# Performance work log

Measured on AMD Instinct MI355X. Metric: run time of the kernel, lower is better.

Reference implementation:

```python
import jax, jax.numpy as jnp
import numpy as np

# Per-species MLP dims from CoefficientLayer._create_model (H, C, N, O), aev_dim=384
DIMS = {"h": [384, 160, 128, 96, 1], "c": [384, 144, 112, 96, 1], "n": [384, 128, 112, 96, 1], "o": [384, 128, 112, 96, 1]}


def setup_inputs() -> dict:
    key = jax.random.key(0)
    B, A, D = 256, 256, 384
    ks = jax.random.split(key, 64)
    inp = {}
    inp["species"] = jax.random.randint(ks[0], (B, A), 0, 4)  # species index 0..3
    inp["aev"] = jax.random.normal(ks[1], (B, A, D), dtype=jnp.float32)
    inp["b0"] = jnp.array([0.1, 0.2, 0.3, 0.4], dtype=jnp.float32)  # shifter intercepts
    inp["b1"] = jnp.array([1.0, 1.1, 0.9, 1.2], dtype=jnp.float32)  # shifter slopes
    ki = 2
    for name, dims in DIMS.items():
        for l in range(4):
            fi, fo = dims[l], dims[l + 1]
            inp[f"{name}w{l}"] = jax.random.normal(ks[ki], (fi, fo), dtype=jnp.float32) / np.float32(np.sqrt(fi))
            ki += 1
            inp[f"{name}b{l}"] = jnp.zeros((fo,), dtype=jnp.float32)
    return inp


def _mlp(x, ws, bs):
    # Linear -> CELU(0.1) x3 -> Linear(->1), squeeze last dim
    for i in range(3):
        x = jax.nn.celu(x @ ws[i] + bs[i], alpha=0.1)
    return (x @ ws[3] + bs[3])[..., 0]


def reference(species, aev, b0, b1,
              hw0, hb0, hw1, hb1, hw2, hb2, hw3, hb3,
              cw0, cb0, cw1, cb1, cw2, cb2, cw3, cb3,
              nw0, nb0, nw1, nb1, nw2, nb2, nw3, nb3,
              ow0, ob0, ow1, ob1, ow2, ob2, ow3, ob3):
    nets = [
        ([hw0, hw1, hw2, hw3], [hb0, hb1, hb2, hb3]),
        ([cw0, cw1, cw2, cw3], [cb0, cb1, cb2, cb3]),
        ([nw0, nw1, nw2, nw3], [nb0, nb1, nb2, nb3]),
        ([ow0, ow1, ow2, ow3], [ob0, ob1, ob2, ob3]),
    ]
    # ANIModel hard routing: each atom's coefficient comes from its species' network;
    # atoms with species == -1 (padding) stay 0.
    coef = jnp.zeros(species.shape, dtype=aev.dtype)
    for i, (ws, bs) in enumerate(nets):  # fixed small loop over 4 species
        coef = jnp.where(species == i, _mlp(aev, ws, bs), coef)
    # Shifter: result[mask_i] = b0[i] + b1[i] * coef[mask_i]; padding stays 0
    idx = jnp.clip(species, 0)
    return jnp.where(species >= 0, b0[idx] + b1[idx] * coef, jnp.zeros((), dtype=aev.dtype))
```

## Files before the change

kernel.cpp:

```cpp
#include <hip/hip_runtime.h>

typedef _Float16 f16;
typedef _Float16 f16x4 __attribute__((ext_vector_type(4)));
typedef _Float16 f16x8 __attribute__((ext_vector_type(8)));
typedef float f32x4 __attribute__((ext_vector_type(4)));
typedef unsigned short u16;
typedef unsigned int u32;

#define NATOMS 65536
#define CAP 17920

#define WS_LISTS_OFF 256
#define WS_W_OFF 524544
#define WS_W_ELEMS 350208
#define WS_ACT0_OFF (2u << 20)
#define WS_BIG (46u << 20)

#define BLK0 128
#define BLK12 64

#define ROWB 1536
#define ROWH 768
#define TILEH 12288

struct ConvJob { const float* src; int K, N, KS, NT, CK, off; };

struct PrepParams {
  const int* species;
  int* counts;
  u16* lists;
  f16* wbase;
  ConvJob jobs[16];
};

struct GemmParams {
  const float* aev;
  const float* b0;
  const float* b1;
  const float* bias[4][4];
  const float* w3src[4];
  const f16* w[4][4];
  const int* counts;
  const u16* lists;
  f16* act0;
  float* out;
  int Nreal0[4];
  int Nreal1[4];
};

template <int N> struct AF { f16x8 v[N]; };

__global__ __launch_bounds__(256) void prep_kernel(PrepParams p) {
  int tid = threadIdx.x;
  if (blockIdx.x < 256) {
    __shared__ int wcnt[4][4];
    __shared__ int wbase[4][4];
    int i = blockIdx.x * 256 + tid;
    int s = p.species[i];
    int wave = tid >> 6, lane = tid & 63;
    unsigned long long m[4];
    #pragma unroll
    for (int t = 0; t < 4; t++) {
      m[t] = __ballot(s == t);
      if (lane == 0) wcnt[wave][t] = __popcll(m[t]);
    }
    __syncthreads();
    if (tid < 4) {
      int t = tid;
      int c0 = wcnt[0][t], c1 = wcnt[1][t], c2 = wcnt[2][t], c3 = wcnt[3][t];
      int base = atomicAdd(&p.counts[t], c0 + c1 + c2 + c3);
      wbase[0][t] = base;
      wbase[1][t] = base + c0;
      wbase[2][t] = base + c0 + c1;
      wbase[3][t] = base + c0 + c1 + c2;
    }
    __syncthreads();
    int rnk = __popcll(m[s] & ((1ull << lane) - 1ull));
    p.lists[s * NATOMS + wbase[wave][s] + rnk] = (u16)i;
  } else {
    int bx = blockIdx.x - 256;
    int job = bx / 30, bxin = bx - job * 30;
    ConvJob jb = p.jobs[job];
    int e = bxin * 256 + tid;
    int nslots = jb.KS * jb.NT * 64;
    if (e >= nslots) return;
    int frag = e >> 6, lane = e & 63;
    int c = frag / (jb.CK * jb.NT);
    int rem = frag - c * (jb.CK * jb.NT);
    int ckc = min(jb.CK, jb.KS - c * jb.CK);
    int nt = rem / ckc, ki = rem - nt * ckc;
    int ks = c * jb.CK + ki;
    int q = lane >> 4, nlo = lane & 15;
    int n = nt * 16 + nlo;
    int k0 = ks * 32 + q * 8;
    f16x8 v;
    #pragma unroll
    for (int j = 0; j < 8; j++) {
      int k = k0 + j;
      float x = (n < jb.N && k < jb.K) ? jb.src[k * jb.N + n] : 0.f;
      v[j] = (f16)x;
    }
    *(f16x8*)(p.wbase + jb.off + (size_t)e * 8) = v;
  }
}

__device__ __forceinline__ float celu01(float v) {
  return v > 0.f ? v : 0.1f * (__expf(v * 10.f) - 1.f);
}

__device__ __forceinline__ void stage_frag(const f16* g, f16* l, int lane) {
  __builtin_amdgcn_global_load_lds(
      (const __attribute__((address_space(1))) u32*)(g + lane * 8),
      (__attribute__((address_space(3))) u32*)l, 16, 0, 0);
}

template <int NT0>
__device__ void k0_body(const GemmParams& p, int s, int bl, char* smem) {
  int tid = threadIdx.x, w = tid >> 6, lane = tid & 63;
  int q = lane >> 4, nlo = lane & 15;
  int cnt = min(p.counts[s], CAP);
  int ntiles = (cnt + 15) >> 4;
  int tpb = (ntiles + BLK0 - 1) / BLK0;
  int t0 = bl * tpb;
  int nt_blk = min(ntiles - t0, tpb);
  if (nt_blk <= 0) return;

  const u16* list = p.lists + s * NATOMS;
  u16* atoms_l = (u16*)(smem + 2 * TILEH);

  f16x8 wf[12];
  float bvv[4];
  if (w < NT0) {
    const f16* wg = p.w[s][0];
    #pragma unroll
    for (int ks = 0; ks < 12; ks++)
      wf[ks] = *(const f16x8*)(wg + (size_t)(ks * NT0 + w) * 512 + lane * 8);
    #pragma unroll
    for (int r = 0; r < 4; r++) {
      int n = w * 16 + q * 4 + r;
      bvv[r] = (n < p.Nreal0[s]) ? p.bias[s][0][n] : 0.f;
    }
  }
  f16* act = p.act0 + (size_t)s * CAP * 160;

  for (int idx = tid; idx < nt_blk * 16; idx += 640)
    atoms_l[idx] = list[min(t0 * 16 + idx, cnt - 1)];
  __syncthreads();

  bool stager = (w < 8);
  int frow[3], fintra[3];
  #pragma unroll
  for (int j = 0; j < 3; j++) {
    int o32 = (w + 8 * j) * 1024 + lane * 16;
    frow[j] = o32 / ROWB;
    fintra[j] = o32 - frow[j] * ROWB;
  }

  f32x4 ld[3];
  auto issue = [&](int i) {
    #pragma unroll
    for (int j = 0; j < 3; j++) {
      int atom = atoms_l[i * 16 + frow[j]];
      ld[j] = *(const f32x4*)((const char*)p.aev + (size_t)atom * ROWB + fintra[j]);
    }
  };
  auto write_lds = [&](int i) {
    char* buf = smem + (i & 1) * TILEH;
    #pragma unroll
    for (int j = 0; j < 3; j++) {
      int o16 = (w + 8 * j) * 512 + lane * 8;
      int addr = o16 ^ ((frow[j] & 7) << 4);
      f16x4 h = {(f16)ld[j][0], (f16)ld[j][1], (f16)ld[j][2], (f16)ld[j][3]};
      *(f16x4*)(buf + addr) = h;
    }
  };

  if (stager) {
    issue(0);
    write_lds(0);
    if (nt_blk > 1) issue(1);
  }
  asm volatile("s_waitcnt lgkmcnt(0)" ::: "memory");
  __builtin_amdgcn_s_barrier();

  for (int i = 0; i < nt_blk; i++) {
    if (stager) {
      if (i + 1 < nt_blk) write_lds(i + 1);
      if (i + 2 < nt_blk) issue(i + 2);
    }
    if (w < NT0) {
      const char* buf = smem + (i & 1) * TILEH;
      int swz = (nlo & 7) << 4;
      int base = nlo * ROWH + q * 16;
      f32x4 acc = {0.f, 0.f, 0.f, 0.f};
      #pragma unroll
      for (int ks = 0; ks < 12; ks++) {
        f16x8 a = *(const f16x8*)(buf + ((base + ks * 64) ^ swz));
        acc = __builtin_amdgcn_mfma_f32_16x16x32_f16(wf[ks], a, acc, 0, 0, 0);
      }
      int row = (t0 + i) * 16 + nlo;
      if (row < cnt) {
        f16x4 o;
        #pragma unroll
        for (int r = 0; r < 4; r++) o[r] = (f16)celu01(acc[r] + bvv[r]);
        *(f16x4*)(act + (size_t)row * 160 + w * 16 + q * 4) = o;
      }
    }
    asm volatile("s_waitcnt lgkmcnt(0)" ::: "memory");
    __builtin_amdgcn_s_barrier();
  }
}

__global__ __launch_bounds__(640, 5) void k0_kernel(GemmParams p) {
  __shared__ __align__(16) char smem[2 * TILEH + 384];
  int s = blockIdx.x & 3, bl = blockIdx.x >> 2;
  switch (s) {
    case 0: k0_body<10>(p, 0, bl, smem); break;
    case 1: k0_body<10>(p, 1, bl, smem); break;
    case 2: k0_body<8>(p, 2, bl, smem); break;
    default: k0_body<8>(p, 3, bl, smem); break;
  }
}

template <int KS1>
__device__ void k12_body(const GemmParams& p, int s, int bl, f16* W1, f16* W2,
                         f16* T) {
  int tid = threadIdx.x, w = tid >> 6, lane = tid & 63;
  int q = lane >> 4, nlo = lane & 15;
  constexpr int NF1 = KS1 * 8;
  const f16* g1 = p.w[s][1];
  const f16* g2 = p.w[s][2];
  for (int f = w; f < NF1 + 24; f += 8) {
    if (f < NF1) stage_frag(g1 + (size_t)f * 512, W1 + f * 512, lane);
    else stage_frag(g2 + (size_t)(f - NF1) * 512, W2 + (f - NF1) * 512, lane);
  }
  int cnt = min(p.counts[s], CAP);
  int ntiles = (cnt + 15) >> 4;
  const u16* list = p.lists + s * NATOMS;
  int Nr1 = p.Nreal1[s];
  const float* bias1 = p.bias[s][1];
  const float* bias2 = p.bias[s][2];
  const float* w3 = p.w3src[s];
  float bv[8], b2v[6], w3v[6];
  #pragma unroll
  for (int nt = 0; nt < 8; nt++) {
    int n = nt * 16 + nlo;
    bv[nt] = (n < Nr1) ? bias1[n] : 0.f;
  }
  #pragma unroll
  for (int nt = 0; nt < 6; nt++) {
    int n = nt * 16 + nlo;
    b2v[nt] = bias2[n];
    w3v[nt] = w3[n];
  }
  float b3 = p.bias[s][3][0];
  float b0v = p.b0[s], b1v = p.b1[s];
  const f16* act0 = p.act0 + (size_t)s * CAP * 160;
  f16* Tw = T + (w * 16) * 160;
  __syncthreads();

  auto load_a1 = [&](int t) {
    AF<KS1> a;
    int ar = min(t * 16 + nlo, cnt - 1);
    const f16* ap = act0 + (size_t)ar * 160 + q * 8;
    #pragma unroll
    for (int ks = 0; ks < KS1; ks++)
      a.v[ks] = *(const f16x8*)(ap + ks * 32);
    return a;
  };

  int t = bl * 8 + w;
  if (t >= ntiles) return;
  AF<KS1> a1 = load_a1(t);
  while (true) {
    int tn = t + BLK12 * 8;
    AF<KS1> a1n;
    if (tn < ntiles) a1n = load_a1(tn);
    int tb = t * 16;
    f32x4 acc1[8];
    #pragma unroll
    for (int nt = 0; nt < 8; nt++) acc1[nt] = f32x4{0.f, 0.f, 0.f, 0.f};
    #pragma unroll
    for (int ks = 0; ks < KS1; ks++) {
      #pragma unroll
      for (int nt = 0; nt < 8; nt++) {
        f16x8 b = *(const f16x8*)(W1 + (ks * 8 + nt) * 512 + lane * 8);
        acc1[nt] = __builtin_amdgcn_mfma_f32_16x16x32_f16(a1.v[ks], b, acc1[nt], 0, 0, 0);
      }
    }
    #pragma unroll
    for (int nt = 0; nt < 8; nt++) {
      #pragma unroll
      for (int r = 0; r < 4; r++)
        Tw[(q * 4 + r) * 160 + nt * 16 + nlo] = (f16)celu01(acc1[nt][r] + bv[nt]);
    }
    AF<4> a2;
    #pragma unroll
    for (int ks = 0; ks < 4; ks++)
      a2.v[ks] = *(const f16x8*)(Tw + nlo * 160 + ks * 32 + q * 8);
    f32x4 acc2[6];
    #pragma unroll
    for (int nt = 0; nt < 6; nt++) acc2[nt] = f32x4{0.f, 0.f, 0.f, 0.f};
    #pragma unroll
    for (int ks = 0; ks < 4; ks++) {
      #pragma unroll
      for (int nt = 0; nt < 6; nt++) {
        f16x8 b = *(const f16x8*)(W2 + (ks * 6 + nt) * 512 + lane * 8);
        acc2[nt] = __builtin_amdgcn_mfma_f32_16x16x32_f16(a2.v[ks], b, acc2[nt], 0, 0, 0);
      }
    }
    float pr[4] = {0.f, 0.f, 0.f, 0.f};
    #pragma unroll
    for (int nt = 0; nt < 6; nt++) {
      #pragma unroll
      for (int r = 0; r < 4; r++) {
        float v = celu01(acc2[nt][r] + b2v[nt]);
        pr[r] += v * w3v[nt];
      }
    }
    #pragma unroll
    for (int m = 1; m < 16; m <<= 1) {
      #pragma unroll
      for (int r = 0; r < 4; r++) pr[r] += __shfl_xor(pr[r], m);
    }
    if (nlo == 0) {
      #pragma unroll
      for (int r = 0; r < 4; r++) {
        int row = tb + q * 4 + r;
        if (row < cnt) p.out[list[row]] = b0v + b1v * (pr[r] + b3);
      }
    }
    if (tn >= ntiles) break;
    a1 = a1n;
    t = tn;
  }
}

__global__ __launch_bounds__(512, 2) void k12_kernel(GemmParams p) {
  __shared__ __align__(16) f16 W1[5 * 8 * 512];
  __shared__ __align__(16) f16 W2[4 * 6 * 512];
  __shared__ __align__(16) f16 T[8 * 16 * 160];
  int s = blockIdx.x & 3, bl = blockIdx.x >> 2;
  switch (s) {
    case 0: k12_body<5>(p, 0, bl, W1, W2, T); break;
    case 1: k12_body<5>(p, 1, bl, W1, W2, T); break;
    case 2: k12_body<4>(p, 2, bl, W1, W2, T); break;
    default: k12_body<4>(p, 3, bl, W1, W2, T); break;
  }
}


extern "C" void kernel_launch(void* const* d_in, const int* in_sizes, int n_in,
                              void* d_out, int out_size, void* d_ws, size_t ws_size,
                              hipStream_t stream) {
  if (ws_size < WS_BIG) return;

  const int* species = (const int*)d_in[0];
  const float* aev = (const float*)d_in[1];
  const float* b0 = (const float*)d_in[2];
  const float* b1 = (const float*)d_in[3];

  static const int F1[4]  = {160, 144, 128, 128};
  static const int F1p[4] = {160, 160, 128, 128};
  static const int F2[4]  = {128, 112, 112, 112};

  char* wsb = (char*)d_ws;
  int* counts = (int*)wsb;
  u16* lists = (u16*)(wsb + WS_LISTS_OFF);
  f16* wbase = (f16*)(wsb + WS_W_OFF);

  PrepParams pp;
  pp.species = species; pp.counts = counts; pp.lists = lists; pp.wbase = wbase;

  GemmParams mp;
  mp.aev = aev; mp.b0 = b0; mp.b1 = b1;
  mp.counts = counts; mp.lists = lists; mp.out = (float*)d_out;
  mp.act0 = (f16*)(wsb + WS_ACT0_OFF);

  int off = 0, ji = 0;
  for (int s = 0; s < 4; s++) {
    int K[4]  = {384, F1[s], F2[s], 96};
    int N[4]  = {F1[s], F2[s], 96, 1};
    int KS[4] = {12, F1p[s] / 32, 4, 3};
    int NT[4] = {F1p[s] / 16, 8, 6, 1};
    int CK[4] = {1, 1, 1, 3};
    for (int l = 0; l < 4; l++) {
      const float* w = (const float*)d_in[4 + s * 8 + l * 2];
      const float* b = (const float*)d_in[4 + s * 8 + l * 2 + 1];
      pp.jobs[ji].src = w;
      pp.jobs[ji].K = K[l];
      pp.jobs[ji].N = N[l];
      pp.jobs[ji].KS = KS[l];
      pp.jobs[ji].NT = NT[l];
      pp.jobs[ji].CK = CK[l];
      pp.jobs[ji].off = off;
      mp.w[s][l] = wbase + off;
      mp.bias[s][l] = b;
      off += KS[l] * NT[l] * 512;
      ji++;
    }
    mp.w3src[s] = (const float*)d_in[4 + s * 8 + 6];
    mp.Nreal0[s] = F1[s];
    mp.Nreal1[s] = F2[s];
  }

  hipMemsetAsync(d_ws, 0, 64, stream);
  prep_kernel<<<dim3(256 + 480), 256, 0, stream>>>(pp);
  k0_kernel<<<dim3(4 * BLK0), 640, 0, stream>>>(mp);
  k12_kernel<<<dim3(4 * BLK12), 512, 0, stream>>>(mp);
}
```

Before: 260.3 us.

## Fuse layer-0 GEMM with layers 1-3 into one kernel via LDS activations

Merges the layer-0 kernel and the layers-1/2/3 kernel into one kernel. Layer-0 outputs for up to 8 tiles are kept in LDS, then each wave runs the remaining MLP layers on one tile, so the fp16 activation tensor is no longer written to and read back from global memory and one launch disappears. In exchange, LDS use grows to about 130KB per block, occupancy drops, grid size halves to 64 blocks per species, and the layer-0 aev prefetch pipeline restarts every 8 tiles with extra barriers.

```diff
diff --git a/kernel.cpp b/kernel.cpp
--- a/kernel.cpp
+++ b/kernel.cpp
@@ -13,11 +13,9 @@
 #define WS_LISTS_OFF 256
 #define WS_W_OFF 524544
 #define WS_W_ELEMS 350208
-#define WS_ACT0_OFF (2u << 20)
-#define WS_BIG (46u << 20)
-
-#define BLK0 128
-#define BLK12 64
+#define WS_NEEDED (WS_W_OFF + WS_W_ELEMS * 2)
+
+#define BLKF 64
 
 #define ROWB 1536
 #define ROWH 768
@@ -42,7 +40,6 @@
   const f16* w[4][4];
   const int* counts;
   const u16* lists;
-  f16* act0;
   float* out;
   int Nreal0[4];
   int Nreal1[4];
@@ -114,19 +111,35 @@
       (__attribute__((address_space(3))) u32*)l, 16, 0, 0);
 }
 
-template <int NT0>
-__device__ void k0_body(const GemmParams& p, int s, int bl, char* smem) {
+template <int NT0, int KS1>
+__device__ void fused_body(const GemmParams& p, int s, int bl, char* smem) {
+  constexpr int LDSA_OFF = 2 * TILEH;
+  constexpr int TSTRIDE = 16 * 168;
+  constexpr int W1_OFF = LDSA_OFF + 8 * TSTRIDE * 2;
+  constexpr int W2_OFF = W1_OFF + 40 * 512 * 2;
+  constexpr int ATOMS_OFF = W2_OFF + 24 * 512 * 2;
+  constexpr int NF1 = KS1 * 8;
+
   int tid = threadIdx.x, w = tid >> 6, lane = tid & 63;
   int q = lane >> 4, nlo = lane & 15;
   int cnt = min(p.counts[s], CAP);
   int ntiles = (cnt + 15) >> 4;
-  int tpb = (ntiles + BLK0 - 1) / BLK0;
+  int tpb = (ntiles + BLKF - 1) / BLKF;
   int t0 = bl * tpb;
   int nt_blk = min(ntiles - t0, tpb);
   if (nt_blk <= 0) return;
 
-  const u16* list = p.lists + s * NATOMS;
-  u16* atoms_l = (u16*)(smem + 2 * TILEH);
+  f16* ldsA = (f16*)(smem + LDSA_OFF);
+  f16* W1 = (f16*)(smem + W1_OFF);
+  f16* W2 = (f16*)(smem + W2_OFF);
+  u16* atoms_l = (u16*)(smem + ATOMS_OFF);
+
+  const f16* g1 = p.w[s][1];
+  const f16* g2 = p.w[s][2];
+  for (int f = w; f < NF1 + 24; f += 10) {
+    if (f < NF1) stage_frag(g1 + (size_t)f * 512, W1 + f * 512, lane);
+    else stage_frag(g2 + (size_t)(f - NF1) * 512, W2 + (f - NF1) * 512, lane);
+  }
 
   f16x8 wf[12];
   float bvv[4];
@@ -141,8 +154,27 @@
       bvv[r] = (n < p.Nreal0[s]) ? p.bias[s][0][n] : 0.f;
     }
   }
-  f16* act = p.act0 + (size_t)s * CAP * 160;
-
+
+  int Nr1 = p.Nreal1[s];
+  const float* bias1 = p.bias[s][1];
+  const float* bias2 = p.bias[s][2];
+  const float* w3 = p.w3src[s];
+  float bv1[8], b2v[6], w3v[6];
+  #pragma unroll
+  for (int nt = 0; nt < 8; nt++) {
+    int n = nt * 16 + nlo;
+    bv1[nt] = (n < Nr1) ? bias1[n] : 0.f;
+  }
+  #pragma unroll
+  for (int nt = 0; nt < 6; nt++) {
+    int n = nt * 16 + nlo;
+    b2v[nt] = bias2[n];
+    w3v[nt] = w3[n];
+  }
+  float b3 = p.bias[s][3][0];
+  float b0v = p.b0[s], b1v = p.b1[s];
+
+  const u16* list = p.lists + s * NATOMS;
   for (int idx = tid; idx < nt_blk * 16; idx += 640)
     atoms_l[idx] = list[min(t0 * 16 + idx, cnt - 1)];
   __syncthreads();
@@ -175,177 +207,117 @@
     }
   };
 
-  if (stager) {
-    issue(0);
-    write_lds(0);
-    if (nt_blk > 1) issue(1);
-  }
-  asm volatile("s_waitcnt lgkmcnt(0)" ::: "memory");
-  __builtin_amdgcn_s_barrier();
-
-  for (int i = 0; i < nt_blk; i++) {
+  for (int lo = 0; lo < nt_blk; lo += 8) {
+    int hi = min(nt_blk, lo + 8);
+
     if (stager) {
-      if (i + 1 < nt_blk) write_lds(i + 1);
-      if (i + 2 < nt_blk) issue(i + 2);
-    }
-    if (w < NT0) {
-      const char* buf = smem + (i & 1) * TILEH;
-      int swz = (nlo & 7) << 4;
-      int base = nlo * ROWH + q * 16;
-      f32x4 acc = {0.f, 0.f, 0.f, 0.f};
-      #pragma unroll
-      for (int ks = 0; ks < 12; ks++) {
-        f16x8 a = *(const f16x8*)(buf + ((base + ks * 64) ^ swz));
-        acc = __builtin_amdgcn_mfma_f32_16x16x32_f16(wf[ks], a, acc, 0, 0, 0);
-      }
-      int row = (t0 + i) * 16 + nlo;
-      if (row < cnt) {
-        f16x4 o;
-        #pragma unroll
-        for (int r = 0; r < 4; r++) o[r] = (f16)celu01(acc[r] + bvv[r]);
-        *(f16x4*)(act + (size_t)row * 160 + w * 16 + q * 4) = o;
-      }
+      issue(lo);
+      write_lds(lo);
+      if (lo + 1 < hi) issue(lo + 1);
     }
     asm volatile("s_waitcnt lgkmcnt(0)" ::: "memory");
     __builtin_amdgcn_s_barrier();
-  }
-}
-
-__global__ __launch_bounds__(640, 5) void k0_kernel(GemmParams p) {
-  __shared__ __align__(16) char smem[2 * TILEH + 384];
+
+    for (int i = lo; i < hi; i++) {
+      if (stager) {
+        if (i + 1 < hi) write_lds(i + 1);
+        if (i + 2 < hi) issue(i + 2);
+      }
+      if (w < NT0) {
+        const char* buf = smem + (i & 1) * TILEH;
+        int swz = (nlo & 7) << 4;
+        int base = nlo * ROWH + q * 16;
+        f32x4 acc = {0.f, 0.f, 0.f, 0.f};
+        #pragma unroll
+        for (int ks = 0; ks < 12; ks++) {
+          f16x8 a = *(const f16x8*)(buf + ((base + ks * 64) ^ swz));
+          acc = __builtin_amdgcn_mfma_f32_16x16x32_f16(wf[ks], a, acc, 0, 0, 0);
+        }
+        f16* A = ldsA + (i - lo) * TSTRIDE;
+        f16x4 o;
+        #pragma unroll
+        for (int r = 0; r < 4; r++) o[r] = (f16)celu01(acc[r] + bvv[r]);
+        *(f16x4*)(A + nlo * 168 + w * 16 + q * 4) = o;
+      }
+      asm volatile("s_waitcnt lgkmcnt(0)" ::: "memory");
+      __builtin_amdgcn_s_barrier();
+    }
+
+    if (w < 8 && lo + w < hi) {
+      int i = lo + w;
+      f16* A = ldsA + w * TSTRIDE;
+      AF<KS1> a1;
+      #pragma unroll
+      for (int ks = 0; ks < KS1; ks++)
+        a1.v[ks] = *(const f16x8*)(A + nlo * 168 + ks * 32 + q * 8);
+      f32x4 acc1[8];
+      #pragma unroll
+      for (int nt = 0; nt < 8; nt++) acc1[nt] = f32x4{0.f, 0.f, 0.f, 0.f};
+      #pragma unroll
+      for (int ks = 0; ks < KS1; ks++) {
+        #pragma unroll
+        for (int nt = 0; nt < 8; nt++) {
+          f16x8 b = *(const f16x8*)(W1 + (ks * 8 + nt) * 512 + lane * 8);
+          acc1[nt] = __builtin_amdgcn_mfma_f32_16x16x32_f16(a1.v[ks], b, acc1[nt], 0, 0, 0);
+        }
+      }
+      #pragma unroll
+      for (int nt = 0; nt < 8; nt++) {
+        #pragma unroll
+        for (int r = 0; r < 4; r++)
+          A[(q * 4 + r) * 168 + nt * 16 + nlo] = (f16)celu01(acc1[nt][r] + bv1[nt]);
+      }
+      AF<4> a2;
+      #pragma unroll
+      for (int ks = 0; ks < 4; ks++)
+        a2.v[ks] = *(const f16x8*)(A + nlo * 168 + ks * 32 + q * 8);
+      f32x4 acc2[6];
+      #pragma unroll
+      for (int nt = 0; nt < 6; nt++) acc2[nt] = f32x4{0.f, 0.f, 0.f, 0.f};
+      #pragma unroll
+      for (int ks = 0; ks < 4; ks++) {
+        #pragma unroll
+        for (int nt = 0; nt < 6; nt++) {
+          f16x8 b = *(const f16x8*)(W2 + (ks * 6 + nt) * 512 + lane * 8);
+          acc2[nt] = __builtin_amdgcn_mfma_f32_16x16x32_f16(a2.v[ks], b, acc2[nt], 0, 0, 0);
+        }
+      }
+      float pr[4] = {0.f, 0.f, 0.f, 0.f};
+      #pragma unroll
+      for (int nt = 0; nt < 6; nt++) {
+        #pragma unroll
+        for (int r = 0; r < 4; r++) {
+          float v = celu01(acc2[nt][r] + b2v[nt]);
+          pr[r] += v * w3v[nt];
+        }
+      }
+      #pragma unroll
+      for (int m = 1; m < 16; m <<= 1) {
+        #pragma unroll
+        for (int r = 0; r < 4; r++) pr[r] += __shfl_xor(pr[r], m);
+      }
+      if (nlo == 0) {
+        #pragma unroll
+        for (int r = 0; r < 4; r++) {
+          int row = (t0 + i) * 16 + q * 4 + r;
+          if (row < cnt)
+            p.out[atoms_l[i * 16 + q * 4 + r]] = b0v + b1v * (pr[r] + b3);
+        }
+      }
+    }
+    asm volatile("s_waitcnt lgkmcnt(0)" ::: "memory");
+    __builtin_amdgcn_s_barrier();
+  }
+}
+
+__global__ __launch_bounds__(640, 2) void fused_kernel(GemmParams p) {
+  __shared__ __align__(16) char smem[133760];
   int s = blockIdx.x & 3, bl = blockIdx.x >> 2;
   switch (s) {
-    case 0: k0_body<10>(p, 0, bl, smem); break;
-    case 1: k0_body<10>(p, 1, bl, smem); break;
-    case 2: k0_body<8>(p, 2, bl, smem); break;
-    default: k0_body<8>(p, 3, bl, smem); break;
-  }
-}
-
-template <int KS1>
-__device__ void k12_body(const GemmParams& p, int s, int bl, f16* W1, f16* W2,
-                         f16* T) {
-  int tid = threadIdx.x, w = tid >> 6, lane = tid & 63;
-  int q = lane >> 4, nlo = lane & 15;
-  constexpr int NF1 = KS1 * 8;
-  const f16* g1 = p.w[s][1];
-  const f16* g2 = p.w[s][2];
-  for (int f = w; f < NF1 + 24; f += 8) {
-    if (f < NF1) stage_frag(g1 + (size_t)f * 512, W1 + f * 512, lane);
-    else stage_frag(g2 + (size_t)(f - NF1) * 512, W2 + (f - NF1) * 512, lane);
-  }
-  int cnt = min(p.counts[s], CAP);
-  int ntiles = (cnt + 15) >> 4;
-  const u16* list = p.lists + s * NATOMS;
-  int Nr1 = p.Nreal1[s];
-  const float* bias1 = p.bias[s][1];
-  const float* bias2 = p.bias[s][2];
-  const float* w3 = p.w3src[s];
-  float bv[8], b2v[6], w3v[6];
-  #pragma unroll
-  for (int nt = 0; nt < 8; nt++) {
-    int n = nt * 16 + nlo;
-    bv[nt] = (n < Nr1) ? bias1[n] : 0.f;
-  }
-  #pragma unroll
-  for (int nt = 0; nt < 6; nt++) {
-    int n = nt * 16 + nlo;
-    b2v[nt] = bias2[n];
-    w3v[nt] = w3[n];
-  }
-  float b3 = p.bias[s][3][0];
-  float b0v = p.b0[s], b1v = p.b1[s];
-  const f16* act0 = p.act0 + (size_t)s * CAP * 160;
-  f16* Tw = T + (w * 16) * 160;
-  __syncthreads();
-
-  auto load_a1 = [&](int t) {
-    AF<KS1> a;
-    int ar = min(t * 16 + nlo, cnt - 1);
-    const f16* ap = act0 + (size_t)ar * 160 + q * 8;
-    #pragma unroll
-    for (int ks = 0; ks < KS1; ks++)
-      a.v[ks] = *(const f16x8*)(ap + ks * 32);
-    return a;
-  };
-
-  int t = bl * 8 + w;
-  if (t >= ntiles) return;
-  AF<KS1> a1 = load_a1(t);
-  while (true) {
-    int tn = t + BLK12 * 8;
-    AF<KS1> a1n;
-    if (tn < ntiles) a1n = load_a1(tn);
-    int tb = t * 16;
-    f32x4 acc1[8];
-    #pragma unroll
-    for (int nt = 0; nt < 8; nt++) acc1[nt] = f32x4{0.f, 0.f, 0.f, 0.f};
-    #pragma unroll
-    for (int ks = 0; ks < KS1; ks++) {
-      #pragma unroll
-      for (int nt = 0; nt < 8; nt++) {
-        f16x8 b = *(const f16x8*)(W1 + (ks * 8 + nt) * 512 + lane * 8);
-        acc1[nt] = __builtin_amdgcn_mfma_f32_16x16x32_f16(a1.v[ks], b, acc1[nt], 0, 0, 0);
-      }
-    }
-    #pragma unroll
-    for (int nt = 0; nt < 8; nt++) {
-      #pragma unroll
-      for (int r = 0; r < 4; r++)
-        Tw[(q * 4 + r) * 160 + nt * 16 + nlo] = (f16)celu01(acc1[nt][r] + bv[nt]);
-    }
-    AF<4> a2;
-    #pragma unroll
-    for (int ks = 0; ks < 4; ks++)
-      a2.v[ks] = *(const f16x8*)(Tw + nlo * 160 + ks * 32 + q * 8);
-    f32x4 acc2[6];
-    #pragma unroll
-    for (int nt = 0; nt < 6; nt++) acc2[nt] = f32x4{0.f, 0.f, 0.f, 0.f};
-    #pragma unroll
-    for (int ks = 0; ks < 4; ks++) {
-      #pragma unroll
-      for (int nt = 0; nt < 6; nt++) {
-        f16x8 b = *(const f16x8*)(W2 + (ks * 6 + nt) * 512 + lane * 8);
-        acc2[nt] = __builtin_amdgcn_mfma_f32_16x16x32_f16(a2.v[ks], b, acc2[nt], 0, 0, 0);
-      }
-    }
-    float pr[4] = {0.f, 0.f, 0.f, 0.f};
-    #pragma unroll
-    for (int nt = 0; nt < 6; nt++) {
-      #pragma unroll
-      for (int r = 0; r < 4; r++) {
-        float v = celu01(acc2[nt][r] + b2v[nt]);
-        pr[r] += v * w3v[nt];
-      }
-    }
-    #pragma unroll
-    for (int m = 1; m < 16; m <<= 1) {
-      #pragma unroll
-      for (int r = 0; r < 4; r++) pr[r] += __shfl_xor(pr[r], m);
-    }
-    if (nlo == 0) {
-      #pragma unroll
-      for (int r = 0; r < 4; r++) {
-        int row = tb + q * 4 + r;
-        if (row < cnt) p.out[list[row]] = b0v + b1v * (pr[r] + b3);
-      }
-    }
-    if (tn >= ntiles) break;
-    a1 = a1n;
-    t = tn;
-  }
-}
-
-__global__ __launch_bounds__(512, 2) void k12_kernel(GemmParams p) {
-  __shared__ __align__(16) f16 W1[5 * 8 * 512];
-  __shared__ __align__(16) f16 W2[4 * 6 * 512];
-  __shared__ __align__(16) f16 T[8 * 16 * 160];
-  int s = blockIdx.x & 3, bl = blockIdx.x >> 2;
-  switch (s) {
-    case 0: k12_body<5>(p, 0, bl, W1, W2, T); break;
-    case 1: k12_body<5>(p, 1, bl, W1, W2, T); break;
-    case 2: k12_body<4>(p, 2, bl, W1, W2, T); break;
-    default: k12_body<4>(p, 3, bl, W1, W2, T); break;
+    case 0: fused_body<10, 5>(p, 0, bl, smem); break;
+    case 1: fused_body<10, 5>(p, 1, bl, smem); break;
+    case 2: fused_body<8, 4>(p, 2, bl, smem); break;
+    default: fused_body<8, 4>(p, 3, bl, smem); break;
   }
 }
 
@@ -353,7 +325,7 @@
 extern "C" void kernel_launch(void* const* d_in, const int* in_sizes, int n_in,
                               void* d_out, int out_size, void* d_ws, size_t ws_size,
                               hipStream_t stream) {
-  if (ws_size < WS_BIG) return;
+  if (ws_size < WS_NEEDED) return;
 
   const int* species = (const int*)d_in[0];
   const float* aev = (const float*)d_in[1];
@@ -375,7 +347,6 @@
   GemmParams mp;
   mp.aev = aev; mp.b0 = b0; mp.b1 = b1;
   mp.counts = counts; mp.lists = lists; mp.out = (float*)d_out;
-  mp.act0 = (f16*)(wsb + WS_ACT0_OFF);
 
   int off = 0, ji = 0;
   for (int s = 0; s < 4; s++) {
@@ -406,6 +377,5 @@
 
   hipMemsetAsync(d_ws, 0, 64, stream);
   prep_kernel<<<dim3(256 + 480), 256, 0, stream>>>(pp);
-  k0_kernel<<<dim3(4 * BLK0), 640, 0, stream>>>(mp);
-  k12_kernel<<<dim3(4 * BLK12), 512, 0, stream>>>(mp);
-}
+  fused_kernel<<<dim3(4 * BLKF), 640, 0, stream>>>(mp);
+}
```

After: 246.9 us. -5.1%, faster.
